# Optimization experiments

Hardware: AMD Instinct MI355X
Metric: run time of the kernel (lower is better)

Reference implementation:

```python
import jax, jax.numpy as jnp
import numpy as np

N_NODES = 10000
DEG = 16
E = N_NODES * DEG
IN = 256
OUT = 256
B = 2
SLOPE = 0.2


def setup_inputs() -> dict:
    key = jax.random.key(0)
    ks = jax.random.split(key, 8)
    rng = np.random.default_rng(0)
    # edges sorted by source, every node appears as a source exactly DEG times
    src = np.repeat(np.arange(N_NODES, dtype=np.int64), DEG)
    tgt = rng.integers(0, N_NODES, size=E).astype(np.int64)
    # torch.unique(..., return_inverse=True) -> sorted uniques + inverse ids
    usrc, sid = np.unique(src, return_inverse=True)
    utgt, tid = np.unique(tgt, return_inverse=True)
    s = 1.0 / np.sqrt(IN)
    sa = 1.0 / np.sqrt(2 * OUT)
    return {
        "nodes": jax.random.normal(ks[0], (N_NODES, B, IN), jnp.float32),
        "Ws": jax.random.normal(ks[1], (IN, OUT), jnp.float32) * s,
        "bs": jnp.zeros((OUT,), jnp.float32),
        "Wt": jax.random.normal(ks[2], (IN, OUT), jnp.float32) * s,
        "bt": jnp.zeros((OUT,), jnp.float32),
        "Wv": jax.random.normal(ks[3], (IN, OUT), jnp.float32) * s,
        "bv": jnp.zeros((OUT,), jnp.float32),
        "Wa": jax.random.normal(ks[4], (2 * OUT, 1), jnp.float32) * sa,
        "ba": jnp.zeros((1,), jnp.float32),
        "unique_source_node_id": jnp.asarray(usrc),
        "unique_target_node_id": jnp.asarray(utgt),
        "source_id_per_edge": jnp.asarray(sid),
        "target_id_per_edge": jnp.asarray(tid),
    }


def reference(nodes, Ws, bs, Wt, bt, Wv, bv, Wa, ba,
              unique_source_node_id, unique_target_node_id,
              source_id_per_edge, target_id_per_edge):
    Ns = unique_source_node_id.shape[0]
    # project_node_states
    src_proj = nodes[unique_source_node_id] @ Ws + bs          # [Ns, B, O]
    tgt_proj = nodes[unique_target_node_id] @ Wt + bt          # [Nt, B, O]
    # gather_node_pairs + attention + LeakyReLU
    paired = jnp.concatenate(
        [src_proj[source_id_per_edge], tgt_proj[target_id_per_edge]], axis=-1)  # [E, B, 2O]
    scores = jax.nn.leaky_relu(paired @ Wa + ba, SLOPE)        # [E, B, 1]
    # neighbourhood_softmax: exp(clip) then scatter-add over source segments
    ex = jnp.exp(jnp.clip(scores, -2.0, 2.0))
    denom = jax.ops.segment_sum(ex, source_id_per_edge, num_segments=Ns)
    alpha = ex / denom[source_id_per_edge]                     # [E, B, 1]
    # apply_attention (values_type='new')
    vals = nodes[unique_target_node_id] @ Wv + bv              # [Nt, B, O]
    weighted = alpha * vals[target_id_per_edge]                # [E, B, O]
    # aggregate_neighbours: the original indexes the per-edge weighted values
    # by target_id_per_edge along the EDGE axis (faithfully reproduced), then
    # sums contiguous same-source segments.
    gathered = weighted[target_id_per_edge]                    # [E, B, O]
    agg = jax.ops.segment_sum(gathered, source_id_per_edge, num_segments=Ns)
    # update_sources (update_type='sum'), return_only_source_nodes=True
    return src_proj + agg                                      # [Ns, B, O]
```

## Files before the change

kernel.cpp:

```cpp
#include <hip/hip_runtime.h>

#define B2 2
#define DEG 16
#define SLOPE 0.2f

typedef __attribute__((ext_vector_type(8))) short short8;
typedef __attribute__((ext_vector_type(8))) unsigned short ushort8;
typedef __attribute__((ext_vector_type(4))) unsigned short ushort4v;
typedef __attribute__((ext_vector_type(4))) float f32x4;

__device__ inline unsigned short f2bf(float f) {
  union { float f; unsigned u; } v; v.f = f;
  unsigned r = v.u + 0x7fff + ((v.u >> 16) & 1);
  return (unsigned short)(r >> 16);
}
__device__ inline float bf2f(unsigned short u) {
  union { unsigned u; float f; } c; c.u = ((unsigned)u) << 16;
  return c.f;
}

__device__ inline float wave_dot256(const float* __restrict__ a,
                                    const float* __restrict__ b, int lane) {
  float4 x = *(const float4*)(a + lane * 4);
  float4 y = *(const float4*)(b + lane * 4);
  float v = x.x * y.x + x.y * y.y + x.z * y.z + x.w * y.w;
  #pragma unroll
  for (int off = 32; off; off >>= 1) v += __shfl_down(v, off);
  return v;
}

__global__ __launch_bounds__(256) void prep_w_k(
    const float* __restrict__ Ws, const float* __restrict__ Wt,
    const float* __restrict__ Wv, const float* __restrict__ Wa,
    const float* __restrict__ bs, const float* __restrict__ bt,
    unsigned short* __restrict__ WsT, unsigned short* __restrict__ WvT,
    float* __restrict__ ws_comb, float* __restrict__ wt_comb,
    float* __restrict__ consts) {
  int bx = blockIdx.x;
  if (bx < 32) {
    const float* src = (bx & 16) ? Wv : Ws;
    unsigned short* dst = (bx & 16) ? WvT : WsT;
    int rc = bx & 15;
    int r0 = (rc >> 2) * 64, c0 = (rc & 3) * 64;
    __shared__ float tile[64][65];
    int tr = threadIdx.x >> 6, tc = threadIdx.x & 63;
    #pragma unroll
    for (int i = 0; i < 16; ++i) {
      int r = tr * 16 + i;
      tile[r][tc] = src[(long)(r0 + r) * 256 + c0 + tc];
    }
    __syncthreads();
    #pragma unroll
    for (int i = 0; i < 16; ++i) {
      int r = tr * 16 + i;
      dst[(long)(c0 + r) * 256 + r0 + tc] = f2bf(tile[tc][r]);
    }
  } else {
    int wave = (bx - 32) * 4 + (threadIdx.x >> 6);
    int lane = threadIdx.x & 63;
    if (wave >= 514) return;
    const float *vec, *wa;
    float* dst;
    if (wave < 256)       { vec = Ws + (long)wave * 256;         wa = Wa;       dst = ws_comb + wave; }
    else if (wave < 512)  { vec = Wt + (long)(wave - 256) * 256; wa = Wa + 256; dst = wt_comb + (wave - 256); }
    else if (wave == 512) { vec = bs; wa = Wa;       dst = consts; }
    else                  { vec = bt; wa = Wa + 256; dst = consts + 1; }
    float v = wave_dot256(vec, wa, lane);
    if (lane == 0) *dst = v;
  }
}

__global__ __launch_bounds__(256) void prep_nodes_k(
    const float* __restrict__ nodes, const float* __restrict__ ws_comb,
    const float* __restrict__ wt_comb, unsigned short* __restrict__ nodes_bf,
    float* __restrict__ an_s, float* __restrict__ an_t, int nrows) {
  int wave = blockIdx.x * 4 + (threadIdx.x >> 6);
  int lane = threadIdx.x & 63;
  if (wave >= nrows) return;
  const float4 a = *(const float4*)(nodes + (long)wave * 256 + lane * 4);
  ushort4v p;
  p[0] = f2bf(a.x); p[1] = f2bf(a.y); p[2] = f2bf(a.z); p[3] = f2bf(a.w);
  *(ushort4v*)(nodes_bf + (long)wave * 256 + lane * 4) = p;
  const float4 w1 = *(const float4*)(ws_comb + lane * 4);
  const float4 w2 = *(const float4*)(wt_comb + lane * 4);
  float vs = a.x * w1.x + a.y * w1.y + a.z * w1.z + a.w * w1.w;
  float vt = a.x * w2.x + a.y * w2.y + a.z * w2.z + a.w * w2.w;
  #pragma unroll
  for (int off = 32; off; off >>= 1) {
    vs += __shfl_down(vs, off);
    vt += __shfl_down(vt, off);
  }
  if (lane == 0) { an_s[wave] = vs; an_t[wave] = vt; }
}

__global__ __launch_bounds__(256, 2) void gemm_mfma_k(
    const unsigned short* __restrict__ Abf,
    const int* __restrict__ usrc, const int* __restrict__ utgt,
    const unsigned short* __restrict__ WsT, const unsigned short* __restrict__ WvT,
    const float* __restrict__ bs, const float* __restrict__ bv,
    unsigned short* __restrict__ sproj_bf, unsigned short* __restrict__ vals_bf,
    const float* __restrict__ an_s, const float* __restrict__ an_t,
    const int* __restrict__ tid_arr, const float* __restrict__ consts,
    const float* __restrict__ ba, float* __restrict__ alpha,
    int Ms, int Mt, int Ns) {
  if (blockIdx.z == 2) {
    if (blockIdx.y != 0) return;
    int g = blockIdx.x * 256 + threadIdx.x;
    int s = g >> 1, b = g & 1;
    if (s >= Ns) return;
    float base = an_s[(long)usrc[s] * B2 + b] + consts[0] + consts[1] + ba[0];
    float ex[DEG];
    float den = 0.f;
    #pragma unroll
    for (int j = 0; j < DEG; ++j) {
      int t = tid_arr[s * DEG + j];
      float sc = base + an_t[(long)utgt[t] * B2 + b];
      sc = sc > 0.f ? sc : SLOPE * sc;
      sc = fminf(2.f, fmaxf(-2.f, sc));
      float ev = __expf(sc);
      ex[j] = ev;
      den += ev;
    }
    float inv = 1.f / den;
    #pragma unroll
    for (int j = 0; j < DEG; ++j) alpha[(long)(s * DEG + j) * B2 + b] = ex[j] * inv;
    return;
  }
  bool second = blockIdx.z != 0;
  const int* idx = second ? utgt : usrc;
  const unsigned short* WT = second ? WvT : WsT;
  const float* bias = second ? bv : bs;
  unsigned short* dstC = second ? vals_bf : sproj_bf;
  int M = second ? Mt : Ms;
  int row0 = blockIdx.x * 128, col0 = blockIdx.y * 128;
  if (row0 >= M) return;

  constexpr int LDT = 72;
  __shared__ unsigned short As[128 * LDT];
  __shared__ unsigned short Bs[128 * LDT];
  int t = threadIdx.x;
  int wv = t >> 6, lane = t & 63;
  int srow = t >> 3;
  int scol = (t & 7) * 8;
  const unsigned short* ap[4];
  #pragma unroll
  for (int p = 0; p < 4; ++p) {
    int m = row0 + srow + 32 * p;
    int mc = m < M ? m : M - 1;
    long ar = (long)idx[mc >> 1] * B2 + (mc & 1);
    ap[p] = Abf + ar * 256 + scol;
  }
  const unsigned short* bp[4];
  #pragma unroll
  for (int q = 0; q < 4; ++q)
    bp[q] = WT + (long)(col0 + srow + 32 * q) * 256 + scol;

  f32x4 acc[2][8];
  #pragma unroll
  for (int i = 0; i < 2; ++i)
    #pragma unroll
    for (int j = 0; j < 8; ++j) acc[i][j] = (f32x4)(0.f);

  ushort8 av[4], bvv[4];
  #pragma unroll
  for (int p = 0; p < 4; ++p) av[p] = *(const ushort8*)(ap[p]);
  #pragma unroll
  for (int q = 0; q < 4; ++q) bvv[q] = *(const ushort8*)(bp[q]);

  #pragma unroll
  for (int k0 = 0; k0 < 256; k0 += 64) {
    __syncthreads();
    #pragma unroll
    for (int p = 0; p < 4; ++p)
      *(ushort8*)&As[(srow + 32 * p) * LDT + scol] = av[p];
    #pragma unroll
    for (int q = 0; q < 4; ++q)
      *(ushort8*)&Bs[(srow + 32 * q) * LDT + scol] = bvv[q];
    __syncthreads();
    if (k0 < 192) {
      #pragma unroll
      for (int p = 0; p < 4; ++p) av[p] = *(const ushort8*)(ap[p] + k0 + 64);
      #pragma unroll
      for (int q = 0; q < 4; ++q) bvv[q] = *(const ushort8*)(bp[q] + k0 + 64);
    }
    #pragma unroll
    for (int ks = 0; ks < 64; ks += 32) {
      int ko = ks + (lane >> 4) * 8;
      short8 af0 = *(const short8*)&As[(32 * wv + (lane & 15)) * LDT + ko];
      short8 af1 = *(const short8*)&As[(32 * wv + 16 + (lane & 15)) * LDT + ko];
      #pragma unroll
      for (int j = 0; j < 8; ++j) {
        short8 bf = *(const short8*)&Bs[(16 * j + (lane & 15)) * LDT + ko];
        acc[0][j] = __builtin_amdgcn_mfma_f32_16x16x32_bf16(bf, af0, acc[0][j], 0, 0, 0);
        acc[1][j] = __builtin_amdgcn_mfma_f32_16x16x32_bf16(bf, af1, acc[1][j], 0, 0, 0);
      }
    }
  }
  int cq = lane >> 4, rl = lane & 15;
  #pragma unroll
  for (int j = 0; j < 8; ++j) {
    int col = col0 + 16 * j + 4 * cq;
    float4 b4 = *(const float4*)(bias + col);
    #pragma unroll
    for (int i = 0; i < 2; ++i) {
      int row = row0 + 32 * wv + 16 * i + rl;
      if (row < M) {
        ushort4v p;
        p[0] = f2bf(acc[i][j][0] + b4.x);
        p[1] = f2bf(acc[i][j][1] + b4.y);
        p[2] = f2bf(acc[i][j][2] + b4.z);
        p[3] = f2bf(acc[i][j][3] + b4.w);
        *(ushort4v*)(dstC + (long)row * 256 + col) = p;
      }
    }
  }
}

__global__ __launch_bounds__(256) void aggregate_k(
    const unsigned short* __restrict__ sproj, const unsigned short* __restrict__ vals,
    const float* __restrict__ alpha, const int* __restrict__ tid_arr,
    float* __restrict__ out, int Ns) {
  int s = blockIdx.x * 4 + (threadIdx.x >> 6);
  int lane = threadIdx.x & 63;
  if (s >= Ns) return;
  int f = tid_arr[s * DEG + (lane & 15)];
  int b = lane >> 5;
  float al = alpha[(long)f * B2 + b];
  int t2 = tid_arr[f];
  ushort8 sp = __builtin_nontemporal_load(
      (const ushort8*)(sproj + (long)s * 512 + lane * 8));
  float acc[8];
  #pragma unroll
  for (int k = 0; k < 8; ++k) acc[k] = bf2f(sp[k]);
  #pragma unroll
  for (int j = 0; j < DEG; ++j) {
    int rr = __shfl(t2, j);
    float aj = __shfl(al, (lane & 32) + j);
    ushort8 v = *(const ushort8*)(vals + (long)rr * 512 + lane * 8);
    #pragma unroll
    for (int k = 0; k < 8; ++k) acc[k] += aj * bf2f(v[k]);
  }
  long ob = (long)s * 512 + lane * 8;
  f32x4 p0, p1;
  p0[0] = acc[0]; p0[1] = acc[1]; p0[2] = acc[2]; p0[3] = acc[3];
  p1[0] = acc[4]; p1[1] = acc[5]; p1[2] = acc[6]; p1[3] = acc[7];
  __builtin_nontemporal_store(p0, (f32x4*)(out + ob));
  __builtin_nontemporal_store(p1, (f32x4*)(out + ob + 4));
}

extern "C" void kernel_launch(void* const* d_in, const int* in_sizes, int n_in,
                              void* d_out, int out_size, void* d_ws, size_t ws_size,
                              hipStream_t stream) {
  const float* nodes = (const float*)d_in[0];
  const float* Ws = (const float*)d_in[1];
  const float* bs = (const float*)d_in[2];
  const float* Wt = (const float*)d_in[3];
  const float* bt = (const float*)d_in[4];
  const float* Wv = (const float*)d_in[5];
  const float* bv = (const float*)d_in[6];
  const float* Wa = (const float*)d_in[7];
  const float* ba = (const float*)d_in[8];
  const int* usrc = (const int*)d_in[9];
  const int* utgt = (const int*)d_in[10];
  const int* tidp = (const int*)d_in[12];
  int Ns = in_sizes[9], Nt = in_sizes[10];
  int NsB = Ns * B2, NtB = Nt * B2;
  long nrows = in_sizes[0] / 256;

  unsigned short* nodes_bf = (unsigned short*)d_ws;
  unsigned short* WsT = nodes_bf + nrows * 256;
  unsigned short* WvT = WsT + 65536;
  unsigned short* vals_bf = WvT + 65536;
  unsigned short* sproj_bf = vals_bf + (size_t)NtB * 256;
  float* fbase = (float*)(sproj_bf + (size_t)NsB * 256);
  float* an_s = fbase;
  float* an_t = an_s + nrows;
  float* ws_comb = an_t + nrows;
  float* wt_comb = ws_comb + 256;
  float* consts = wt_comb + 256;
  float* alpha = consts + 16;
  float* out = (float*)d_out;

  prep_w_k<<<161, 256, 0, stream>>>(Ws, Wt, Wv, Wa, bs, bt,
                                    WsT, WvT, ws_comb, wt_comb, consts);
  prep_nodes_k<<<(int)((nrows + 3) / 4), 256, 0, stream>>>(
      nodes, ws_comb, wt_comb, nodes_bf, an_s, an_t, (int)nrows);
  int maxM = NsB > NtB ? NsB : NtB;
  gemm_mfma_k<<<dim3((maxM + 127) / 128, 2, 3), 256, 0, stream>>>(
      nodes_bf, usrc, utgt, WsT, WvT, bs, bv, sproj_bf, vals_bf,
      an_s, an_t, tidp, consts, ba, alpha, NsB, NtB, Ns);
  aggregate_k<<<(Ns + 3) / 4, 256, 0, stream>>>(
      sproj_bf, vals_bf, alpha, tidp, out, Ns);
}
```

Baseline: 128.9 us.

## Stage full weight tile in LDS and load A fragments directly from global

The GEMM stage now loads the entire 128x256 weight slice into shared memory once, with padded stride, and reads the gathered activation rows straight from global memory into MFMA operand registers. This removes the per-k-step double-buffered LDS staging of A and B and most of the barriers. The trade-offs are a larger LDS footprint (about 66 KB), which may lower occupancy, an un-overlapped upfront weight load, and less coalesced direct global reads of A.

```diff
diff --git a/kernel.cpp b/kernel.cpp
--- a/kernel.cpp
+++ b/kernel.cpp
@@ -135,25 +135,30 @@
   int row0 = blockIdx.x * 128, col0 = blockIdx.y * 128;
   if (row0 >= M) return;
 
-  constexpr int LDT = 72;
-  __shared__ unsigned short As[128 * LDT];
-  __shared__ unsigned short Bs[128 * LDT];
+  constexpr int LDB = 264;
+  __shared__ unsigned short Bs[128 * LDB];
   int t = threadIdx.x;
+  {
+    const unsigned short* wbase = WT + (long)col0 * 256;
+    #pragma unroll
+    for (int i = 0; i < 32; ++i) {
+      int c = i * 256 + t;
+      int row = c >> 5;
+      int colc = (c & 31) * 8;
+      *(ushort8*)&Bs[row * LDB + colc] =
+          *(const ushort8*)(wbase + (long)row * 256 + colc);
+    }
+  }
   int wv = t >> 6, lane = t & 63;
-  int srow = t >> 3;
-  int scol = (t & 7) * 8;
-  const unsigned short* ap[4];
-  #pragma unroll
-  for (int p = 0; p < 4; ++p) {
-    int m = row0 + srow + 32 * p;
-    int mc = m < M ? m : M - 1;
-    long ar = (long)idx[mc >> 1] * B2 + (mc & 1);
-    ap[p] = Abf + ar * 256 + scol;
-  }
-  const unsigned short* bp[4];
-  #pragma unroll
-  for (int q = 0; q < 4; ++q)
-    bp[q] = WT + (long)(col0 + srow + 32 * q) * 256 + scol;
+  int rl = lane & 15, ko8 = (lane >> 4) * 8;
+  int m0 = row0 + 32 * wv + rl;
+  int m1 = m0 + 16;
+  int mc0 = m0 < M ? m0 : M - 1;
+  int mc1 = m1 < M ? m1 : M - 1;
+  const unsigned short* pA0 =
+      Abf + ((long)idx[mc0 >> 1] * B2 + (mc0 & 1)) * 256 + ko8;
+  const unsigned short* pA1 =
+      Abf + ((long)idx[mc1 >> 1] * B2 + (mc1 & 1)) * 256 + ko8;
 
   f32x4 acc[2][8];
   #pragma unroll
@@ -161,42 +166,19 @@
     #pragma unroll
     for (int j = 0; j < 8; ++j) acc[i][j] = (f32x4)(0.f);
 
-  ushort8 av[4], bvv[4];
-  #pragma unroll
-  for (int p = 0; p < 4; ++p) av[p] = *(const ushort8*)(ap[p]);
-  #pragma unroll
-  for (int q = 0; q < 4; ++q) bvv[q] = *(const ushort8*)(bp[q]);
-
-  #pragma unroll
-  for (int k0 = 0; k0 < 256; k0 += 64) {
-    __syncthreads();
-    #pragma unroll
-    for (int p = 0; p < 4; ++p)
-      *(ushort8*)&As[(srow + 32 * p) * LDT + scol] = av[p];
-    #pragma unroll
-    for (int q = 0; q < 4; ++q)
-      *(ushort8*)&Bs[(srow + 32 * q) * LDT + scol] = bvv[q];
-    __syncthreads();
-    if (k0 < 192) {
-      #pragma unroll
-      for (int p = 0; p < 4; ++p) av[p] = *(const ushort8*)(ap[p] + k0 + 64);
-      #pragma unroll
-      for (int q = 0; q < 4; ++q) bvv[q] = *(const ushort8*)(bp[q] + k0 + 64);
-    }
-    #pragma unroll
-    for (int ks = 0; ks < 64; ks += 32) {
-      int ko = ks + (lane >> 4) * 8;
-      short8 af0 = *(const short8*)&As[(32 * wv + (lane & 15)) * LDT + ko];
-      short8 af1 = *(const short8*)&As[(32 * wv + 16 + (lane & 15)) * LDT + ko];
-      #pragma unroll
-      for (int j = 0; j < 8; ++j) {
-        short8 bf = *(const short8*)&Bs[(16 * j + (lane & 15)) * LDT + ko];
-        acc[0][j] = __builtin_amdgcn_mfma_f32_16x16x32_bf16(bf, af0, acc[0][j], 0, 0, 0);
-        acc[1][j] = __builtin_amdgcn_mfma_f32_16x16x32_bf16(bf, af1, acc[1][j], 0, 0, 0);
-      }
-    }
-  }
-  int cq = lane >> 4, rl = lane & 15;
+  __syncthreads();
+  #pragma unroll
+  for (int k0 = 0; k0 < 256; k0 += 32) {
+    short8 af0 = *(const short8*)(pA0 + k0);
+    short8 af1 = *(const short8*)(pA1 + k0);
+    #pragma unroll
+    for (int j = 0; j < 8; ++j) {
+      short8 bf = *(const short8*)&Bs[(16 * j + rl) * LDB + k0 + ko8];
+      acc[0][j] = __builtin_amdgcn_mfma_f32_16x16x32_bf16(bf, af0, acc[0][j], 0, 0, 0);
+      acc[1][j] = __builtin_amdgcn_mfma_f32_16x16x32_bf16(bf, af1, acc[1][j], 0, 0, 0);
+    }
+  }
+  int cq = lane >> 4;
   #pragma unroll
   for (int j = 0; j < 8; ++j) {
     int col = col0 + 16 * j + 4 * cq;
```

After: 134.6 us. 1.04x slower.

## Fuse four launches into one persistent cooperative kernel with grid syncs

Applied to the files above, without the earlier changes.

Replaces the four-kernel pipeline (weight prep, node bf16 conversion, MFMA GEMM plus softmax, aggregation) with one cooperative kernel of 512 blocks. The stages are separated by grid-wide syncs and each stage walks its work units in a grid-stride loop. The aim is to remove per-launch overhead and the gaps between dependent launches. The costs are grid-barrier latency, fixed occupancy at two blocks per CU, and a fallback to the old kernels if the cooperative launch fails.

```diff
diff --git a/kernel.cpp b/kernel.cpp
--- a/kernel.cpp
+++ b/kernel.cpp
@@ -1,4 +1,7 @@
 #include <hip/hip_runtime.h>
+#include <hip/hip_cooperative_groups.h>
+
+namespace cg = cooperative_groups;
 
 #define B2 2
 #define DEG 16
@@ -27,6 +30,243 @@
   #pragma unroll
   for (int off = 32; off; off >>= 1) v += __shfl_down(v, off);
   return v;
+}
+
+union SMemU {
+  float tile[64][65];
+  struct { unsigned short As[128 * 72], Bs[128 * 72]; } g;
+};
+
+__global__ __launch_bounds__(256, 2) void fused_k(
+    const float* __restrict__ nodes, const float* __restrict__ Ws,
+    const float* __restrict__ bs, const float* __restrict__ Wt,
+    const float* __restrict__ bt, const float* __restrict__ Wv,
+    const float* __restrict__ bv, const float* __restrict__ Wa,
+    const float* __restrict__ ba, const int* __restrict__ usrc,
+    const int* __restrict__ utgt, const int* __restrict__ tidp,
+    unsigned short* __restrict__ nodes_bf, unsigned short* __restrict__ WsT,
+    unsigned short* __restrict__ WvT, unsigned short* __restrict__ vals_bf,
+    unsigned short* __restrict__ sproj_bf, float* __restrict__ an_s,
+    float* __restrict__ an_t, float* __restrict__ ws_comb,
+    float* __restrict__ wt_comb, float* __restrict__ consts,
+    float* __restrict__ alpha, float* __restrict__ out,
+    int Ms, int Mt, int Ns, int nrows) {
+  __shared__ SMemU sm;
+  const int tix = threadIdx.x;
+  const int nb = gridDim.x;
+
+  for (int u = blockIdx.x; u < 161; u += nb) {
+    if (u < 32) {
+      const float* src = (u & 16) ? Wv : Ws;
+      unsigned short* dst = (u & 16) ? WvT : WsT;
+      int rc = u & 15;
+      int r0 = (rc >> 2) * 64, c0 = (rc & 3) * 64;
+      int tr = tix >> 6, tc = tix & 63;
+      #pragma unroll
+      for (int i = 0; i < 16; ++i) {
+        int r = tr * 16 + i;
+        sm.tile[r][tc] = src[(long)(r0 + r) * 256 + c0 + tc];
+      }
+      __syncthreads();
+      #pragma unroll
+      for (int i = 0; i < 16; ++i) {
+        int r = tr * 16 + i;
+        dst[(long)(c0 + r) * 256 + r0 + tc] = f2bf(sm.tile[tc][r]);
+      }
+      __syncthreads();
+    } else {
+      int wave = (u - 32) * 4 + (tix >> 6);
+      int lane = tix & 63;
+      if (wave < 514) {
+        const float *vec, *wa;
+        float* dst;
+        if (wave < 256)       { vec = Ws + (long)wave * 256;         wa = Wa;       dst = ws_comb + wave; }
+        else if (wave < 512)  { vec = Wt + (long)(wave - 256) * 256; wa = Wa + 256; dst = wt_comb + (wave - 256); }
+        else if (wave == 512) { vec = bs; wa = Wa;       dst = consts; }
+        else                  { vec = bt; wa = Wa + 256; dst = consts + 1; }
+        float v = wave_dot256(vec, wa, lane);
+        if (lane == 0) *dst = v;
+      }
+    }
+  }
+  __threadfence();
+  cg::this_grid().sync();
+
+  int nP1 = (nrows + 3) >> 2;
+  for (int u = blockIdx.x; u < nP1; u += nb) {
+    int row = u * 4 + (tix >> 6);
+    int lane = tix & 63;
+    if (row < nrows) {
+      const float4 a = *(const float4*)(nodes + (long)row * 256 + lane * 4);
+      ushort4v p;
+      p[0] = f2bf(a.x); p[1] = f2bf(a.y); p[2] = f2bf(a.z); p[3] = f2bf(a.w);
+      *(ushort4v*)(nodes_bf + (long)row * 256 + lane * 4) = p;
+      const float4 w1 = *(const float4*)(ws_comb + lane * 4);
+      const float4 w2 = *(const float4*)(wt_comb + lane * 4);
+      float vs = a.x * w1.x + a.y * w1.y + a.z * w1.z + a.w * w1.w;
+      float vt = a.x * w2.x + a.y * w2.y + a.z * w2.z + a.w * w2.w;
+      #pragma unroll
+      for (int off = 32; off; off >>= 1) {
+        vs += __shfl_down(vs, off);
+        vt += __shfl_down(vt, off);
+      }
+      if (lane == 0) { an_s[row] = vs; an_t[row] = vt; }
+    }
+  }
+  __threadfence();
+  cg::this_grid().sync();
+
+  int maxM = Ms > Mt ? Ms : Mt;
+  int nx = (maxM + 127) >> 7;
+  int ngemm = 4 * nx;
+  int nsm = (Ns * B2 + 255) >> 8;
+  for (int u = blockIdx.x; u < ngemm + nsm; u += nb) {
+    if (u < ngemm) {
+      int z = u / (2 * nx);
+      int rem = u - z * 2 * nx;
+      int y = rem / nx;
+      int x = rem - y * nx;
+      bool second = z != 0;
+      const int* idx = second ? utgt : usrc;
+      const unsigned short* WT = second ? WvT : WsT;
+      const float* bias = second ? bv : bs;
+      unsigned short* dstC = second ? vals_bf : sproj_bf;
+      int M = second ? Mt : Ms;
+      int row0 = x * 128, col0 = y * 128;
+      if (row0 < M) {
+        constexpr int LDT = 72;
+        int wv = tix >> 6, lane = tix & 63;
+        int srow = tix >> 3, scol = (tix & 7) * 8;
+        const unsigned short* ap[4];
+        #pragma unroll
+        for (int p = 0; p < 4; ++p) {
+          int m = row0 + srow + 32 * p;
+          int mc = m < M ? m : M - 1;
+          long ar = (long)idx[mc >> 1] * B2 + (mc & 1);
+          ap[p] = nodes_bf + ar * 256 + scol;
+        }
+        const unsigned short* bp[4];
+        #pragma unroll
+        for (int q = 0; q < 4; ++q)
+          bp[q] = WT + (long)(col0 + srow + 32 * q) * 256 + scol;
+
+        f32x4 acc[2][8];
+        #pragma unroll
+        for (int i = 0; i < 2; ++i)
+          #pragma unroll
+          for (int j = 0; j < 8; ++j) acc[i][j] = (f32x4)(0.f);
+
+        ushort8 av[4], bvv[4];
+        #pragma unroll
+        for (int p = 0; p < 4; ++p) av[p] = *(const ushort8*)(ap[p]);
+        #pragma unroll
+        for (int q = 0; q < 4; ++q) bvv[q] = *(const ushort8*)(bp[q]);
+
+        #pragma unroll
+        for (int k0 = 0; k0 < 256; k0 += 64) {
+          __syncthreads();
+          #pragma unroll
+          for (int p = 0; p < 4; ++p)
+            *(ushort8*)&sm.g.As[(srow + 32 * p) * LDT + scol] = av[p];
+          #pragma unroll
+          for (int q = 0; q < 4; ++q)
+            *(ushort8*)&sm.g.Bs[(srow + 32 * q) * LDT + scol] = bvv[q];
+          __syncthreads();
+          if (k0 < 192) {
+            #pragma unroll
+            for (int p = 0; p < 4; ++p) av[p] = *(const ushort8*)(ap[p] + k0 + 64);
+            #pragma unroll
+            for (int q = 0; q < 4; ++q) bvv[q] = *(const ushort8*)(bp[q] + k0 + 64);
+          }
+          #pragma unroll
+          for (int ks = 0; ks < 64; ks += 32) {
+            int ko = ks + (lane >> 4) * 8;
+            short8 af0 = *(const short8*)&sm.g.As[(32 * wv + (lane & 15)) * LDT + ko];
+            short8 af1 = *(const short8*)&sm.g.As[(32 * wv + 16 + (lane & 15)) * LDT + ko];
+            #pragma unroll
+            for (int j = 0; j < 8; ++j) {
+              short8 bf = *(const short8*)&sm.g.Bs[(16 * j + (lane & 15)) * LDT + ko];
+              acc[0][j] = __builtin_amdgcn_mfma_f32_16x16x32_bf16(bf, af0, acc[0][j], 0, 0, 0);
+              acc[1][j] = __builtin_amdgcn_mfma_f32_16x16x32_bf16(bf, af1, acc[1][j], 0, 0, 0);
+            }
+          }
+        }
+        int cq = lane >> 4, rl = lane & 15;
+        #pragma unroll
+        for (int j = 0; j < 8; ++j) {
+          int col = col0 + 16 * j + 4 * cq;
+          float4 b4 = *(const float4*)(bias + col);
+          #pragma unroll
+          for (int i = 0; i < 2; ++i) {
+            int row = row0 + 32 * wv + 16 * i + rl;
+            if (row < M) {
+              ushort4v p;
+              p[0] = f2bf(acc[i][j][0] + b4.x);
+              p[1] = f2bf(acc[i][j][1] + b4.y);
+              p[2] = f2bf(acc[i][j][2] + b4.z);
+              p[3] = f2bf(acc[i][j][3] + b4.w);
+              *(ushort4v*)(dstC + (long)row * 256 + col) = p;
+            }
+          }
+        }
+      }
+    } else {
+      int g = (u - ngemm) * 256 + tix;
+      int s = g >> 1, b = g & 1;
+      if (s < Ns) {
+        float base = an_s[(long)usrc[s] * B2 + b] + consts[0] + consts[1] + ba[0];
+        float ex[DEG];
+        float den = 0.f;
+        #pragma unroll
+        for (int j = 0; j < DEG; ++j) {
+          int t = tidp[s * DEG + j];
+          float sc = base + an_t[(long)utgt[t] * B2 + b];
+          sc = sc > 0.f ? sc : SLOPE * sc;
+          sc = fminf(2.f, fmaxf(-2.f, sc));
+          float ev = __expf(sc);
+          ex[j] = ev;
+          den += ev;
+        }
+        float inv = 1.f / den;
+        #pragma unroll
+        for (int j = 0; j < DEG; ++j)
+          alpha[(long)(s * DEG + j) * B2 + b] = ex[j] * inv;
+      }
+    }
+  }
+  __threadfence();
+  cg::this_grid().sync();
+
+  int nP3 = (Ns + 3) >> 2;
+  for (int u = blockIdx.x; u < nP3; u += nb) {
+    int s = u * 4 + (tix >> 6);
+    int lane = tix & 63;
+    if (s < Ns) {
+      int f = tidp[s * DEG + (lane & 15)];
+      int b = lane >> 5;
+      float al = alpha[(long)f * B2 + b];
+      int t2 = tidp[f];
+      ushort8 sp = __builtin_nontemporal_load(
+          (const ushort8*)(sproj_bf + (long)s * 512 + lane * 8));
+      float acc[8];
+      #pragma unroll
+      for (int k = 0; k < 8; ++k) acc[k] = bf2f(sp[k]);
+      #pragma unroll
+      for (int j = 0; j < DEG; ++j) {
+        int rr = __shfl(t2, j);
+        float aj = __shfl(al, (lane & 32) + j);
+        ushort8 v = *(const ushort8*)(vals_bf + (long)rr * 512 + lane * 8);
+        #pragma unroll
+        for (int k = 0; k < 8; ++k) acc[k] += aj * bf2f(v[k]);
+      }
+      long ob = (long)s * 512 + lane * 8;
+      f32x4 p0, p1;
+      p0[0] = acc[0]; p0[1] = acc[1]; p0[2] = acc[2]; p0[3] = acc[3];
+      p1[0] = acc[4]; p1[1] = acc[5]; p1[2] = acc[6]; p1[3] = acc[7];
+      __builtin_nontemporal_store(p0, (f32x4*)(out + ob));
+      __builtin_nontemporal_store(p1, (f32x4*)(out + ob + 4));
+    }
+  }
 }
 
 __global__ __launch_bounds__(256) void prep_w_k(
@@ -266,6 +506,7 @@
   int Ns = in_sizes[9], Nt = in_sizes[10];
   int NsB = Ns * B2, NtB = Nt * B2;
   long nrows = in_sizes[0] / 256;
+  int nrowsi = (int)nrows;
 
   unsigned short* nodes_bf = (unsigned short*)d_ws;
   unsigned short* WsT = nodes_bf + nrows * 256;
@@ -281,14 +522,26 @@
   float* alpha = consts + 16;
   float* out = (float*)d_out;
 
-  prep_w_k<<<161, 256, 0, stream>>>(Ws, Wt, Wv, Wa, bs, bt,
-                                    WsT, WvT, ws_comb, wt_comb, consts);
-  prep_nodes_k<<<(int)((nrows + 3) / 4), 256, 0, stream>>>(
-      nodes, ws_comb, wt_comb, nodes_bf, an_s, an_t, (int)nrows);
-  int maxM = NsB > NtB ? NsB : NtB;
-  gemm_mfma_k<<<dim3((maxM + 127) / 128, 2, 3), 256, 0, stream>>>(
-      nodes_bf, usrc, utgt, WsT, WvT, bs, bv, sproj_bf, vals_bf,
-      an_s, an_t, tidp, consts, ba, alpha, NsB, NtB, Ns);
-  aggregate_k<<<(Ns + 3) / 4, 256, 0, stream>>>(
-      sproj_bf, vals_bf, alpha, tidp, out, Ns);
-}
+  void* args[] = {
+      (void*)&nodes, (void*)&Ws, (void*)&bs, (void*)&Wt, (void*)&bt,
+      (void*)&Wv, (void*)&bv, (void*)&Wa, (void*)&ba, (void*)&usrc,
+      (void*)&utgt, (void*)&tidp, (void*)&nodes_bf, (void*)&WsT,
+      (void*)&WvT, (void*)&vals_bf, (void*)&sproj_bf, (void*)&an_s,
+      (void*)&an_t, (void*)&ws_comb, (void*)&wt_comb, (void*)&consts,
+      (void*)&alpha, (void*)&out, (void*)&NsB, (void*)&NtB, (void*)&Ns,
+      (void*)&nrowsi};
+  hipError_t err = hipLaunchCooperativeKernel(
+      (const void*)fused_k, dim3(512), dim3(256), (void**)args, 0, stream);
+  if (err != hipSuccess) {
+    prep_w_k<<<161, 256, 0, stream>>>(Ws, Wt, Wv, Wa, bs, bt,
+                                      WsT, WvT, ws_comb, wt_comb, consts);
+    prep_nodes_k<<<(int)((nrows + 3) / 4), 256, 0, stream>>>(
+        nodes, ws_comb, wt_comb, nodes_bf, an_s, an_t, (int)nrows);
+    int maxM = NsB > NtB ? NsB : NtB;
+    gemm_mfma_k<<<dim3((maxM + 127) / 128, 2, 3), 256, 0, stream>>>(
+        nodes_bf, usrc, utgt, WsT, WvT, bs, bv, sproj_bf, vals_bf,
+        an_s, an_t, tidp, consts, ba, alpha, NsB, NtB, Ns);
+    aggregate_k<<<(Ns + 3) / 4, 256, 0, stream>>>(
+        sproj_bf, vals_bf, alpha, tidp, out, Ns);
+  }
+}
```

Measured after the change: 494.2 us. 283% more time.
